# Kernel tuning notes

Measured on AMD Instinct MI355X. Metric: run time of the kernel, lower is better.

The kernel has to match this reference:

```python
import jax, jax.numpy as jnp
import numpy as np

D_MODEL = 512
NHEAD = 8


def setup_inputs() -> dict:
    key = jax.random.key(0)
    k0, k1, k2 = jax.random.split(key, 3)
    s = 1.0 / np.sqrt(D_MODEL)  # torch default uniform init bound (xavier-ish)
    return {
        "x": jax.random.normal(k0, (2, 4096, D_MODEL), dtype=jnp.float32),
        "in_proj_w": jax.random.uniform(k1, (3 * D_MODEL, D_MODEL), jnp.float32, -s, s),
        "in_proj_b": jnp.zeros((3 * D_MODEL,), jnp.float32),
        "out_proj_w": jax.random.uniform(k2, (D_MODEL, D_MODEL), jnp.float32, -s, s),
        "out_proj_b": jnp.zeros((D_MODEL,), jnp.float32),
        "window_size": 128,
    }


def reference(x, in_proj_w, in_proj_b, out_proj_w, out_proj_b, window_size):
    # Faithful to nn.MultiheadAttention (eval mode, dropout inactive).
    # NOTE: PyTorch bool attn_mask: True = disallowed. The module sets True
    # INSIDE the window, so in-window positions are masked OUT.
    B, S, D = x.shape
    H = NHEAD
    hd = D // H

    qkv = x @ in_proj_w.T + in_proj_b                      # [B,S,3D]
    q, k, v = jnp.split(qkv, 3, axis=-1)
    q = q.reshape(B, S, H, hd).transpose(0, 2, 1, 3)       # [B,H,S,hd]
    k = k.reshape(B, S, H, hd).transpose(0, 2, 1, 3)
    v = v.reshape(B, S, H, hd).transpose(0, 2, 1, 3)

    scores = jnp.einsum('bhqd,bhkd->bhqk', q, k) / jnp.sqrt(jnp.float32(hd))

    idx = jnp.arange(S)
    in_window = jnp.abs(idx[:, None] - idx[None, :]) <= window_size  # [S,S]
    scores = jnp.where(in_window, -jnp.inf, scores)

    attn = jax.nn.softmax(scores, axis=-1)                 # [B,H,S,S]
    ctx = jnp.einsum('bhqk,bhkd->bhqd', attn, v)           # [B,H,S,hd]
    ctx = ctx.transpose(0, 2, 1, 3).reshape(B, S, D)       # [B,S,D]
    return ctx @ out_proj_w.T + out_proj_b
```

## Files before the change

### kernel.cpp

```cpp
#include <hip/hip_runtime.h>
#include <hip/hip_bf16.h>

typedef unsigned short u16;
typedef __bf16 bf16x8 __attribute__((ext_vector_type(8)));
typedef short s16x4 __attribute__((ext_vector_type(4)));
typedef float f32x4 __attribute__((ext_vector_type(4)));

__device__ __forceinline__ f32x4 mfma16(bf16x8 a, bf16x8 b, f32x4 c) {
    return __builtin_amdgcn_mfma_f32_16x16x32_bf16(a, b, c, 0, 0, 0);
}
__device__ __forceinline__ f32x4 mfma16k16(s16x4 a, s16x4 b, f32x4 c) {
    return __builtin_amdgcn_mfma_f32_16x16x16bf16_1k(a, b, c, 0, 0, 0);
}

__device__ __forceinline__ u16 f2b(float x) {
    union { float f; unsigned u; } a; a.f = x;
    unsigned r = a.u + 0x7fffu + ((a.u >> 16) & 1u);
    return (u16)(r >> 16);
}

__global__ __launch_bounds__(256) void k_cast(const float* __restrict__ src,
                                              u16* __restrict__ dst, int n) {
    int i = (blockIdx.x * 256 + threadIdx.x) * 4;
    if (i >= n) return;
    float4 f = *(const float4*)&src[i];
    u16 o[4] = { f2b(f.x), f2b(f.y), f2b(f.z), f2b(f.w) };
    *(uint2*)&dst[i] = *(uint2*)o;
}

__global__ __launch_bounds__(256) void k_gemm_qkv(const u16* __restrict__ xb,
                                                  const u16* __restrict__ wb,
                                                  const float* __restrict__ bias,
                                                  u16* __restrict__ qkvout) {
    __shared__ u16 As[128][40];
    __shared__ u16 Ws[128][40];
    const int tid = threadIdx.x;
    const int w = tid >> 6, lane = tid & 63, l15 = lane & 15, quad = lane >> 4;
    const int mb = blockIdx.x * 128, nb = blockIdx.y * 128;

    f32x4 acc[2][8];
#pragma unroll
    for (int i = 0; i < 2; i++)
#pragma unroll
        for (int j = 0; j < 8; j++) acc[i][j] = (f32x4){0.f, 0.f, 0.f, 0.f};

    for (int k0 = 0; k0 < 512; k0 += 32) {
        {
            int row = tid >> 1, cc = (tid & 1) * 16;
            const u16* g = &xb[(size_t)(mb + row) * 512 + k0 + cc];
            *(uint4*)&As[row][cc]     = *(const uint4*)g;
            *(uint4*)&As[row][cc + 8] = *(const uint4*)(g + 8);
            const u16* gw = &wb[(size_t)(nb + row) * 512 + k0 + cc];
            *(uint4*)&Ws[row][cc]     = *(const uint4*)gw;
            *(uint4*)&Ws[row][cc + 8] = *(const uint4*)(gw + 8);
        }
        __syncthreads();
        bf16x8 a0 = *(const bf16x8*)&As[w * 32 + l15][quad * 8];
        bf16x8 a1 = *(const bf16x8*)&As[w * 32 + 16 + l15][quad * 8];
#pragma unroll
        for (int nt = 0; nt < 8; nt++) {
            bf16x8 bfr = *(const bf16x8*)&Ws[nt * 16 + l15][quad * 8];
            acc[0][nt] = mfma16(a0, bfr, acc[0][nt]);
            acc[1][nt] = mfma16(a1, bfr, acc[1][nt]);
        }
        __syncthreads();
    }
    const int seg = nb >> 9;
    u16* obase = qkvout + (size_t)seg * (16ull * 4096 * 64);
    if (seg < 2) {
        const float sc = (seg == 0) ? 0.125f * 1.44269504088896340736f : 1.0f;
#pragma unroll
        for (int mt = 0; mt < 2; mt++)
#pragma unroll
            for (int nt = 0; nt < 8; nt++) {
                int dcol = nb + nt * 16 + l15;
                int hh = (dcol >> 6) & 7, dloc = dcol & 63;
                float bs = bias[dcol];
#pragma unroll
                for (int r = 0; r < 4; r++) {
                    int m = mb + w * 32 + mt * 16 + quad * 4 + r;
                    float vv = (acc[mt][nt][r] + bs) * sc;
                    int b = m >> 12, s = m & 4095;
                    obase[((size_t)((b * 8 + hh) * 4096 + s)) * 64 + dloc] = f2b(vv);
                }
            }
    } else {
#pragma unroll
        for (int mt = 0; mt < 2; mt++)
#pragma unroll
            for (int nt = 0; nt < 8; nt++) {
                int dcol = nb + nt * 16 + l15;
                int hh = (dcol >> 6) & 7, dloc = dcol & 63;
                float bs = bias[dcol];
                int m0 = mb + w * 32 + mt * 16 + quad * 4;
                int b = m0 >> 12, s0 = m0 & 4095;
                u16 o[4];
#pragma unroll
                for (int r = 0; r < 4; r++) o[r] = f2b(acc[mt][nt][r] + bs);
                *(uint2*)&obase[((size_t)((b * 8 + hh) * 64 + dloc)) * 4096 + s0] = *(uint2*)o;
            }
    }
}

__global__ __launch_bounds__(128, 2) void k_attn(const u16* __restrict__ qkv,
                                                 u16* __restrict__ ctx,
                                                 const int* __restrict__ win) {
    __shared__ u16 Ks[64][72];
    __shared__ u16 Vt[64][72];
    const int tid = threadIdx.x;
    const int w = tid >> 6, lane = tid & 63, l15 = lane & 15, quad = lane >> 4;
    const int bh = blockIdx.y;
    const int qb0 = blockIdx.x * 64;
    const int W = win[0];
    const u16* qg = qkv;
    const u16* kg = qkv + 16ull * 4096 * 64;
    const u16* vg = qkv + 32ull * 4096 * 64;
    const size_t bhb = (size_t)bh * 4096 * 64;

    bf16x8 qf[2][2];
#pragma unroll
    for (int g = 0; g < 2; g++) {
        const u16* qrow = &qg[bhb + (size_t)(qb0 + w * 32 + g * 16 + l15) * 64];
        qf[g][0] = *(const bf16x8*)&qrow[quad * 8];
        qf[g][1] = *(const bf16x8*)&qrow[32 + quad * 8];
    }

    f32x4 O[2][4];
#pragma unroll
    for (int g = 0; g < 2; g++)
#pragma unroll
        for (int mb = 0; mb < 4; mb++) O[g][mb] = (f32x4){0.f, 0.f, 0.f, 0.f};
    float lsum[2] = {0.f, 0.f};

    const int srow = tid >> 1, shalf = (tid & 1) * 32;
    const u16* kgr = &kg[bhb + (size_t)srow * 64 + shalf];
    const u16* vgr = &vg[((size_t)bh * 64 + srow) * 4096 + shalf];

    for (int kb = 0; kb < 4096; kb += 64) {
        if (max(qb0 + 63 - kb, kb + 63 - qb0) <= W) continue;
        bool partial = (kb + 63 >= qb0 - W) && (kb <= qb0 + 63 + W);
        {
            const u16* kp = kgr + (size_t)kb * 64;
            *(uint4*)&Ks[srow][shalf]      = *(const uint4*)kp;
            *(uint4*)&Ks[srow][shalf + 8]  = *(const uint4*)(kp + 8);
            *(uint4*)&Ks[srow][shalf + 16] = *(const uint4*)(kp + 16);
            *(uint4*)&Ks[srow][shalf + 24] = *(const uint4*)(kp + 24);
            const u16* vp = vgr + kb;
            *(uint4*)&Vt[srow][shalf]      = *(const uint4*)vp;
            *(uint4*)&Vt[srow][shalf + 8]  = *(const uint4*)(vp + 8);
            *(uint4*)&Vt[srow][shalf + 16] = *(const uint4*)(vp + 16);
            *(uint4*)&Vt[srow][shalf + 24] = *(const uint4*)(vp + 24);
        }
        __syncthreads();
        bf16x8 kf[4][2];
#pragma unroll
        for (int nt = 0; nt < 4; nt++) {
            kf[nt][0] = *(const bf16x8*)&Ks[nt * 16 + l15][quad * 8];
            kf[nt][1] = *(const bf16x8*)&Ks[nt * 16 + l15][32 + quad * 8];
        }
        s16x4 vf[4][4];
#pragma unroll
        for (int mb = 0; mb < 4; mb++)
#pragma unroll
            for (int nt = 0; nt < 4; nt++)
                vf[mb][nt] = *(const s16x4*)&Vt[mb * 16 + l15][nt * 16 + quad * 4];
#pragma unroll
        for (int g = 0; g < 2; g++) {
            f32x4 C[4];
#pragma unroll
            for (int nt = 0; nt < 4; nt++) {
                f32x4 z = (f32x4){0.f, 0.f, 0.f, 0.f};
                C[nt] = mfma16(kf[nt][0], qf[g][0], z);
                C[nt] = mfma16(kf[nt][1], qf[g][1], C[nt]);
            }
            s16x4 pb[4];
            if (!partial) {
#pragma unroll
                for (int nt = 0; nt < 4; nt++)
#pragma unroll
                    for (int r = 0; r < 4; r++) {
                        float p = __builtin_amdgcn_exp2f(C[nt][r]);
                        lsum[g] += p;
                        pb[nt][r] = (short)f2b(p);
                    }
            } else {
                int qr = qb0 + w * 32 + g * 16 + l15;
#pragma unroll
                for (int nt = 0; nt < 4; nt++)
#pragma unroll
                    for (int r = 0; r < 4; r++) {
                        int key = kb + nt * 16 + quad * 4 + r;
                        int dd = qr - key; dd = dd < 0 ? -dd : dd;
                        float p = (dd <= W) ? 0.f : __builtin_amdgcn_exp2f(C[nt][r]);
                        lsum[g] += p;
                        pb[nt][r] = (short)f2b(p);
                    }
            }
#pragma unroll
            for (int nt = 0; nt < 4; nt++)
#pragma unroll
                for (int mb = 0; mb < 4; mb++)
                    O[g][mb] = mfma16k16(vf[mb][nt], pb[nt], O[g][mb]);
        }
        __syncthreads();
    }
#pragma unroll
    for (int g = 0; g < 2; g++) {
        lsum[g] += __shfl_xor(lsum[g], 16);
        lsum[g] += __shfl_xor(lsum[g], 32);
    }
    int b = bh >> 3, h = bh & 7;
#pragma unroll
    for (int g = 0; g < 2; g++) {
        float inv = 1.0f / lsum[g];
        int qr = qb0 + w * 32 + g * 16 + l15;
        size_t rowoff = ((size_t)(b * 4096 + qr)) * 512 + h * 64;
#pragma unroll
        for (int mb = 0; mb < 4; mb++) {
            u16 o[4];
#pragma unroll
            for (int r = 0; r < 4; r++) o[r] = f2b(O[g][mb][r] * inv);
            *(uint2*)&ctx[rowoff + mb * 16 + quad * 4] = *(uint2*)o;
        }
    }
}

__global__ __launch_bounds__(256) void k_gemm_out(const u16* __restrict__ ab,
                                                  const u16* __restrict__ wb,
                                                  const float* __restrict__ bias,
                                                  float* __restrict__ out) {
    __shared__ u16 As[128][40];
    __shared__ u16 Ws[128][40];
    const int tid = threadIdx.x;
    const int w = tid >> 6, lane = tid & 63, l15 = lane & 15, quad = lane >> 4;
    const int mb = blockIdx.x * 128, nb = blockIdx.y * 128;

    f32x4 acc[2][8];
#pragma unroll
    for (int i = 0; i < 2; i++)
#pragma unroll
        for (int j = 0; j < 8; j++) acc[i][j] = (f32x4){0.f, 0.f, 0.f, 0.f};

    for (int k0 = 0; k0 < 512; k0 += 32) {
        {
            int row = tid >> 1, cc = (tid & 1) * 16;
            const u16* g = &ab[(size_t)(mb + row) * 512 + k0 + cc];
            *(uint4*)&As[row][cc]     = *(const uint4*)g;
            *(uint4*)&As[row][cc + 8] = *(const uint4*)(g + 8);
            const u16* gw = &wb[(size_t)(nb + row) * 512 + k0 + cc];
            *(uint4*)&Ws[row][cc]     = *(const uint4*)gw;
            *(uint4*)&Ws[row][cc + 8] = *(const uint4*)(gw + 8);
        }
        __syncthreads();
        bf16x8 a0 = *(const bf16x8*)&As[w * 32 + l15][quad * 8];
        bf16x8 a1 = *(const bf16x8*)&As[w * 32 + 16 + l15][quad * 8];
#pragma unroll
        for (int nt = 0; nt < 8; nt++) {
            bf16x8 bfr = *(const bf16x8*)&Ws[nt * 16 + l15][quad * 8];
            acc[0][nt] = mfma16(a0, bfr, acc[0][nt]);
            acc[1][nt] = mfma16(a1, bfr, acc[1][nt]);
        }
        __syncthreads();
    }
#pragma unroll
    for (int mt = 0; mt < 2; mt++)
#pragma unroll
        for (int nt = 0; nt < 8; nt++) {
            int n = nb + nt * 16 + l15;
            float bs = bias[n];
#pragma unroll
            for (int r = 0; r < 4; r++) {
                int m = mb + w * 32 + mt * 16 + quad * 4 + r;
                out[(size_t)m * 512 + n] = acc[mt][nt][r] + bs;
            }
        }
}

extern "C" void kernel_launch(void* const* d_in, const int* in_sizes, int n_in,
                              void* d_out, int out_size, void* d_ws, size_t ws_size,
                              hipStream_t stream) {
    const float* x    = (const float*)d_in[0];
    const float* wqkv = (const float*)d_in[1];
    const float* bqkv = (const float*)d_in[2];
    const float* wout = (const float*)d_in[3];
    const float* bout = (const float*)d_in[4];
    const int*   win  = (const int*)d_in[5];
    float* out = (float*)d_out;

    u16* xb    = (u16*)d_ws;
    u16* wqkvb = xb    + 8192ull * 512;
    u16* woutb = wqkvb + 1536ull * 512;
    u16* qkvb  = woutb + 512ull * 512;
    u16* ctxb  = qkvb  + 3ull * 16 * 4096 * 64;

    k_cast<<<4096, 256, 0, stream>>>(x, xb, 8192 * 512);
    k_cast<<<768, 256, 0, stream>>>(wqkv, wqkvb, 1536 * 512);
    k_cast<<<256, 256, 0, stream>>>(wout, woutb, 512 * 512);
    k_gemm_qkv<<<dim3(64, 12), 256, 0, stream>>>(xb, wqkvb, bqkv, qkvb);
    k_attn<<<dim3(64, 16), 128, 0, stream>>>(qkvb, ctxb, win);
    k_gemm_out<<<dim3(64, 4), 256, 0, stream>>>(ctxb, woutb, bout, out);
}
```

Baseline: 240.2 us.

## Pre-swizzle V into MFMA fragment layout, double-buffer K, fuse casts, retile out GEMM

The QKV GEMM now writes V directly in the per-lane MFMA fragment order, so the attention kernel loads V fragments straight from global memory into registers and no longer stages V in shared memory. K staging becomes a double-buffered, XOR-swizzled shared tile, which allows dropping the trailing barrier in each key-block iteration. The three cast launches are merged into one kernel, bf16 packing switches to paired conversion intrinsics, and the output GEMM uses 64-wide N tiles to launch twice as many blocks. Fetching V per iteration directly from global memory adds load latency and raises register pressure in the attention loop.

```diff
diff --git a/kernel.cpp b/kernel.cpp
--- a/kernel.cpp
+++ b/kernel.cpp
@@ -18,14 +18,29 @@
     unsigned r = a.u + 0x7fffu + ((a.u >> 16) & 1u);
     return (u16)(r >> 16);
 }
-
-__global__ __launch_bounds__(256) void k_cast(const float* __restrict__ src,
-                                              u16* __restrict__ dst, int n) {
+__device__ __forceinline__ unsigned f2b2(float a, float b) {
+    union { __hip_bfloat162 h; unsigned u; } cv;
+    cv.h = __float22bfloat162_rn(make_float2(a, b));
+    return cv.u;
+}
+
+#define NX  (8192 * 512)
+#define NWQ (1536 * 512)
+#define NWO (512 * 512)
+__global__ __launch_bounds__(256) void k_cast_all(const float* __restrict__ x,
+                                                  const float* __restrict__ wq,
+                                                  const float* __restrict__ wo,
+                                                  u16* __restrict__ xb,
+                                                  u16* __restrict__ wqb,
+                                                  u16* __restrict__ wob) {
     int i = (blockIdx.x * 256 + threadIdx.x) * 4;
-    if (i >= n) return;
-    float4 f = *(const float4*)&src[i];
-    u16 o[4] = { f2b(f.x), f2b(f.y), f2b(f.z), f2b(f.w) };
-    *(uint2*)&dst[i] = *(uint2*)o;
+    const float* s; u16* d; int off;
+    if (i < NX)            { s = x;  d = xb;  off = i; }
+    else if (i < NX + NWQ) { s = wq; d = wqb; off = i - NX; }
+    else                   { s = wo; d = wob; off = i - NX - NWQ; }
+    float4 f = *(const float4*)&s[off];
+    uint2 o = make_uint2(f2b2(f.x, f.y), f2b2(f.z, f.w));
+    *(uint2*)&d[off] = o;
 }
 
 __global__ __launch_bounds__(256) void k_gemm_qkv(const u16* __restrict__ xb,
@@ -89,24 +104,27 @@
         for (int mt = 0; mt < 2; mt++)
 #pragma unroll
             for (int nt = 0; nt < 8; nt++) {
-                int dcol = nb + nt * 16 + l15;
-                int hh = (dcol >> 6) & 7, dloc = dcol & 63;
-                float bs = bias[dcol];
+                int c = nb + nt * 16 + l15;
+                int hh = (c >> 6) & 7, d = c & 63;
+                int mbv = d >> 4, l15v = d & 15;
+                float bs = bias[c];
                 int m0 = mb + w * 32 + mt * 16 + quad * 4;
-                int b = m0 >> 12, s0 = m0 & 4095;
-                u16 o[4];
-#pragma unroll
-                for (int r = 0; r < 4; r++) o[r] = f2b(acc[mt][nt][r] + bs);
-                *(uint2*)&obase[((size_t)((b * 8 + hh) * 64 + dloc)) * 4096 + s0] = *(uint2*)o;
+                int b = m0 >> 12, si = m0 & 4095;
+                int kt = si >> 6, ka = si & 63;
+                int ntv = ka >> 4;
+                uint2 o = make_uint2(f2b2(acc[mt][nt][0] + bs, acc[mt][nt][1] + bs),
+                                     f2b2(acc[mt][nt][2] + bs, acc[mt][nt][3] + bs));
+                size_t F4 = ((((((size_t)(b * 8 + hh) * 64 + kt) * 4 + ntv) * 4 + mbv) * 4 + quad) * 16 + l15v);
+                *(uint2*)&obase[F4 * 4] = o;
             }
     }
 }
 
 __global__ __launch_bounds__(128, 2) void k_attn(const u16* __restrict__ qkv,
+                                                 const u16* __restrict__ vfg,
                                                  u16* __restrict__ ctx,
                                                  const int* __restrict__ win) {
-    __shared__ u16 Ks[64][72];
-    __shared__ u16 Vt[64][72];
+    __shared__ u16 Ks[2][64][64];
     const int tid = threadIdx.x;
     const int w = tid >> 6, lane = tid & 63, l15 = lane & 15, quad = lane >> 4;
     const int bh = blockIdx.y;
@@ -114,7 +132,6 @@
     const int W = win[0];
     const u16* qg = qkv;
     const u16* kg = qkv + 16ull * 4096 * 64;
-    const u16* vg = qkv + 32ull * 4096 * 64;
     const size_t bhb = (size_t)bh * 4096 * 64;
 
     bf16x8 qf[2][2];
@@ -132,38 +149,42 @@
         for (int mb = 0; mb < 4; mb++) O[g][mb] = (f32x4){0.f, 0.f, 0.f, 0.f};
     float lsum[2] = {0.f, 0.f};
 
-    const int srow = tid >> 1, shalf = (tid & 1) * 32;
-    const u16* kgr = &kg[bhb + (size_t)srow * 64 + shalf];
-    const u16* vgr = &vg[((size_t)bh * 64 + srow) * 4096 + shalf];
-
+    const int srow = tid >> 1, half = tid & 1, sw = srow & 7;
+    const u16* kgr = &kg[bhb + (size_t)srow * 64 + half * 32];
+    const u16* vb0 = vfg + (size_t)bh * 64 * 4096 + lane * 4;
+
+    int it = 0;
     for (int kb = 0; kb < 4096; kb += 64) {
         if (max(qb0 + 63 - kb, kb + 63 - qb0) <= W) continue;
         bool partial = (kb + 63 >= qb0 - W) && (kb <= qb0 + 63 + W);
+        int p = it & 1; it++;
+        const u16* vt0 = vb0 + (size_t)(kb >> 6) * 4096;
+        const u16* vt1 = vt0 + 2048;
+        s16x4 vfr[16];
+#pragma unroll
+        for (int f = 0; f < 8; f++) vfr[f]     = *(const s16x4*)&vt0[f * 256];
+#pragma unroll
+        for (int f = 0; f < 8; f++) vfr[f + 8] = *(const s16x4*)&vt1[f * 256];
         {
             const u16* kp = kgr + (size_t)kb * 64;
-            *(uint4*)&Ks[srow][shalf]      = *(const uint4*)kp;
-            *(uint4*)&Ks[srow][shalf + 8]  = *(const uint4*)(kp + 8);
-            *(uint4*)&Ks[srow][shalf + 16] = *(const uint4*)(kp + 16);
-            *(uint4*)&Ks[srow][shalf + 24] = *(const uint4*)(kp + 24);
-            const u16* vp = vgr + kb;
-            *(uint4*)&Vt[srow][shalf]      = *(const uint4*)vp;
-            *(uint4*)&Vt[srow][shalf + 8]  = *(const uint4*)(vp + 8);
-            *(uint4*)&Vt[srow][shalf + 16] = *(const uint4*)(vp + 16);
-            *(uint4*)&Vt[srow][shalf + 24] = *(const uint4*)(vp + 24);
+            uint4 kr0 = *(const uint4*)kp;
+            uint4 kr1 = *(const uint4*)(kp + 8);
+            uint4 kr2 = *(const uint4*)(kp + 16);
+            uint4 kr3 = *(const uint4*)(kp + 24);
+            int cb = half * 4;
+            *(uint4*)&Ks[p][srow][((cb + 0) ^ sw) * 8] = kr0;
+            *(uint4*)&Ks[p][srow][((cb + 1) ^ sw) * 8] = kr1;
+            *(uint4*)&Ks[p][srow][((cb + 2) ^ sw) * 8] = kr2;
+            *(uint4*)&Ks[p][srow][((cb + 3) ^ sw) * 8] = kr3;
         }
         __syncthreads();
         bf16x8 kf[4][2];
+        const int rs = l15 & 7;
 #pragma unroll
         for (int nt = 0; nt < 4; nt++) {
-            kf[nt][0] = *(const bf16x8*)&Ks[nt * 16 + l15][quad * 8];
-            kf[nt][1] = *(const bf16x8*)&Ks[nt * 16 + l15][32 + quad * 8];
-        }
-        s16x4 vf[4][4];
-#pragma unroll
-        for (int mb = 0; mb < 4; mb++)
-#pragma unroll
-            for (int nt = 0; nt < 4; nt++)
-                vf[mb][nt] = *(const s16x4*)&Vt[mb * 16 + l15][nt * 16 + quad * 4];
+            kf[nt][0] = *(const bf16x8*)&Ks[p][nt * 16 + l15][(quad ^ rs) * 8];
+            kf[nt][1] = *(const bf16x8*)&Ks[p][nt * 16 + l15][((quad + 4) ^ rs) * 8];
+        }
 #pragma unroll
         for (int g = 0; g < 2; g++) {
             f32x4 C[4];
@@ -176,33 +197,39 @@
             s16x4 pb[4];
             if (!partial) {
 #pragma unroll
-                for (int nt = 0; nt < 4; nt++)
-#pragma unroll
-                    for (int r = 0; r < 4; r++) {
-                        float p = __builtin_amdgcn_exp2f(C[nt][r]);
-                        lsum[g] += p;
-                        pb[nt][r] = (short)f2b(p);
-                    }
+                for (int nt = 0; nt < 4; nt++) {
+                    float p0 = __builtin_amdgcn_exp2f(C[nt][0]);
+                    float p1 = __builtin_amdgcn_exp2f(C[nt][1]);
+                    float p2 = __builtin_amdgcn_exp2f(C[nt][2]);
+                    float p3 = __builtin_amdgcn_exp2f(C[nt][3]);
+                    lsum[g] += (p0 + p1) + (p2 + p3);
+                    union { uint2 u; s16x4 v; } pk;
+                    pk.u = make_uint2(f2b2(p0, p1), f2b2(p2, p3));
+                    pb[nt] = pk.v;
+                }
             } else {
                 int qr = qb0 + w * 32 + g * 16 + l15;
 #pragma unroll
-                for (int nt = 0; nt < 4; nt++)
+                for (int nt = 0; nt < 4; nt++) {
+                    float pv[4];
 #pragma unroll
                     for (int r = 0; r < 4; r++) {
                         int key = kb + nt * 16 + quad * 4 + r;
                         int dd = qr - key; dd = dd < 0 ? -dd : dd;
-                        float p = (dd <= W) ? 0.f : __builtin_amdgcn_exp2f(C[nt][r]);
-                        lsum[g] += p;
-                        pb[nt][r] = (short)f2b(p);
+                        pv[r] = (dd <= W) ? 0.f : __builtin_amdgcn_exp2f(C[nt][r]);
+                        lsum[g] += pv[r];
                     }
+                    union { uint2 u; s16x4 v; } pk;
+                    pk.u = make_uint2(f2b2(pv[0], pv[1]), f2b2(pv[2], pv[3]));
+                    pb[nt] = pk.v;
+                }
             }
 #pragma unroll
             for (int nt = 0; nt < 4; nt++)
 #pragma unroll
                 for (int mb = 0; mb < 4; mb++)
-                    O[g][mb] = mfma16k16(vf[mb][nt], pb[nt], O[g][mb]);
-        }
-        __syncthreads();
+                    O[g][mb] = mfma16k16(vfr[nt * 4 + mb], pb[nt], O[g][mb]);
+        }
     }
 #pragma unroll
     for (int g = 0; g < 2; g++) {
@@ -217,10 +244,9 @@
         size_t rowoff = ((size_t)(b * 4096 + qr)) * 512 + h * 64;
 #pragma unroll
         for (int mb = 0; mb < 4; mb++) {
-            u16 o[4];
-#pragma unroll
-            for (int r = 0; r < 4; r++) o[r] = f2b(O[g][mb][r] * inv);
-            *(uint2*)&ctx[rowoff + mb * 16 + quad * 4] = *(uint2*)o;
+            uint2 o = make_uint2(f2b2(O[g][mb][0] * inv, O[g][mb][1] * inv),
+                                 f2b2(O[g][mb][2] * inv, O[g][mb][3] * inv));
+            *(uint2*)&ctx[rowoff + mb * 16 + quad * 4] = o;
         }
     }
 }
@@ -230,16 +256,16 @@
                                                   const float* __restrict__ bias,
                                                   float* __restrict__ out) {
     __shared__ u16 As[128][40];
-    __shared__ u16 Ws[128][40];
+    __shared__ u16 Ws[64][40];
     const int tid = threadIdx.x;
     const int w = tid >> 6, lane = tid & 63, l15 = lane & 15, quad = lane >> 4;
-    const int mb = blockIdx.x * 128, nb = blockIdx.y * 128;
-
-    f32x4 acc[2][8];
+    const int mb = blockIdx.x * 128, nb = blockIdx.y * 64;
+
+    f32x4 acc[2][4];
 #pragma unroll
     for (int i = 0; i < 2; i++)
 #pragma unroll
-        for (int j = 0; j < 8; j++) acc[i][j] = (f32x4){0.f, 0.f, 0.f, 0.f};
+        for (int j = 0; j < 4; j++) acc[i][j] = (f32x4){0.f, 0.f, 0.f, 0.f};
 
     for (int k0 = 0; k0 < 512; k0 += 32) {
         {
@@ -247,15 +273,14 @@
             const u16* g = &ab[(size_t)(mb + row) * 512 + k0 + cc];
             *(uint4*)&As[row][cc]     = *(const uint4*)g;
             *(uint4*)&As[row][cc + 8] = *(const uint4*)(g + 8);
-            const u16* gw = &wb[(size_t)(nb + row) * 512 + k0 + cc];
-            *(uint4*)&Ws[row][cc]     = *(const uint4*)gw;
-            *(uint4*)&Ws[row][cc + 8] = *(const uint4*)(gw + 8);
+            int wrow = tid >> 2, wcc = (tid & 3) * 8;
+            *(uint4*)&Ws[wrow][wcc] = *(const uint4*)&wb[(size_t)(nb + wrow) * 512 + k0 + wcc];
         }
         __syncthreads();
         bf16x8 a0 = *(const bf16x8*)&As[w * 32 + l15][quad * 8];
         bf16x8 a1 = *(const bf16x8*)&As[w * 32 + 16 + l15][quad * 8];
 #pragma unroll
-        for (int nt = 0; nt < 8; nt++) {
+        for (int nt = 0; nt < 4; nt++) {
             bf16x8 bfr = *(const bf16x8*)&Ws[nt * 16 + l15][quad * 8];
             acc[0][nt] = mfma16(a0, bfr, acc[0][nt]);
             acc[1][nt] = mfma16(a1, bfr, acc[1][nt]);
@@ -265,7 +290,7 @@
 #pragma unroll
     for (int mt = 0; mt < 2; mt++)
 #pragma unroll
-        for (int nt = 0; nt < 8; nt++) {
+        for (int nt = 0; nt < 4; nt++) {
             int n = nb + nt * 16 + l15;
             float bs = bias[n];
 #pragma unroll
@@ -293,10 +318,8 @@
     u16* qkvb  = woutb + 512ull * 512;
     u16* ctxb  = qkvb  + 3ull * 16 * 4096 * 64;
 
-    k_cast<<<4096, 256, 0, stream>>>(x, xb, 8192 * 512);
-    k_cast<<<768, 256, 0, stream>>>(wqkv, wqkvb, 1536 * 512);
-    k_cast<<<256, 256, 0, stream>>>(wout, woutb, 512 * 512);
+    k_cast_all<<<5120, 256, 0, stream>>>(x, wqkv, wout, xb, wqkvb, woutb);
     k_gemm_qkv<<<dim3(64, 12), 256, 0, stream>>>(xb, wqkvb, bqkv, qkvb);
-    k_attn<<<dim3(64, 16), 128, 0, stream>>>(qkvb, ctxb, win);
-    k_gemm_out<<<dim3(64, 4), 256, 0, stream>>>(ctxb, woutb, bout, out);
-}
+    k_attn<<<dim3(64, 16), 128, 0, stream>>>(qkvb, qkvb + 32ull * 4096 * 64, ctxb, win);
+    k_gemm_out<<<dim3(64, 8), 256, 0, stream>>>(ctxb, woutb, bout, out);
+}
```

Measured after the change: 241.4 us. No clear change (+0.5%).
